# Optimization experiments

Measured on AMD Instinct MI355X. Metric: run time of the kernel, lower is better.

The kernel has to match this reference:

```python
import jax, jax.numpy as jnp
import numpy as np

D_MODEL = 1024
D_STATE = 16
DT_RANK = 64  # ceil(1024/16)
DT_MIN, DT_MAX = 1e-3, 1e-1


def setup_inputs() -> dict:
    key = jax.random.key(0)
    ks = jax.random.split(key, 6)
    x = jax.random.normal(ks[0], (2, 2048, D_MODEL), jnp.float32)
    A_log = jax.random.normal(ks[1], (D_MODEL, D_STATE), jnp.float32)
    D = jax.random.normal(ks[2], (D_MODEL,), jnp.float32)
    # nn.Linear default init ~ U(-1/sqrt(fan_in), 1/sqrt(fan_in)); normal*scale is fine for a baseline
    x_proj_w = jax.random.normal(ks[3], (DT_RANK + 2 * D_STATE, D_MODEL), jnp.float32) * (D_MODEL ** -0.5)
    dt_init_std = DT_RANK ** -0.5
    dt_proj_w = jax.random.uniform(ks[4], (D_MODEL, DT_RANK), jnp.float32, -dt_init_std, dt_init_std)
    dt = jnp.exp(jax.random.uniform(ks[5], (D_MODEL,), jnp.float32)
                 * (np.log(DT_MAX) - np.log(DT_MIN)) + np.log(DT_MIN))
    dt_proj_b = dt + jnp.log(-jnp.expm1(-dt))  # inverse-softplus init
    return {"x": x, "A_log": A_log, "D": D, "x_proj_w": x_proj_w,
            "dt_proj_w": dt_proj_w, "dt_proj_b": dt_proj_b}


def _s6(x, A_log, D, x_proj_w, dt_proj_w, dt_proj_b):
    A = -jnp.exp(A_log)                                    # (d, n)
    xp = jnp.einsum('bld,ed->ble', x, x_proj_w)            # (b, l, r+2n)
    d_rank = xp[..., :DT_RANK]
    Bm = xp[..., DT_RANK:DT_RANK + D_STATE]                # (b, l, n)
    Cm = xp[..., DT_RANK + D_STATE:]                       # (b, l, n)
    delta = jax.nn.softplus(jnp.einsum('blr,dr->bld', d_rank, dt_proj_w) + dt_proj_b)
    deltaA = jnp.exp(jnp.einsum('bld,dn->bldn', delta, A))          # (b, l, d, n)
    deltaB_u = jnp.einsum('bld,bln,bld->bldn', delta, Bm, x)        # (b, l, d, n)

    def step(h, inp):
        dA_t, dBu_t, C_t = inp          # (b,d,n), (b,d,n), (b,n)
        h = dA_t * h + dBu_t
        y = jnp.einsum('bdn,bn->bd', h, C_t)
        return h, y

    b, l, d = x.shape
    h0 = jnp.zeros((b, d, D_STATE), x.dtype)
    _, ys = jax.lax.scan(step, h0,
                         (deltaA.transpose(1, 0, 2, 3),
                          deltaB_u.transpose(1, 0, 2, 3),
                          Cm.transpose(1, 0, 2)))
    y = ys.transpose(1, 0, 2) + x * D                      # (b, l, d)
    return y


def reference(x, A_log, D, x_proj_w, dt_proj_w, dt_proj_b):
    return _s6(x, A_log, D, x_proj_w, dt_proj_w, dt_proj_b)
```

## Files before the change

### kernel.cpp

```cpp
#include <hip/hip_runtime.h>
#include <math.h>

#define Bb 2
#define Ll 2048
#define Dm 1024
#define Ns 16
#define Rr 64
#define Ee 96
#define XPS 8
#define BLK (Bb*Ll)
#define NTHR 256
#define LOG2E 1.4426950408889634f
#define LN2   0.6931471805599453f

typedef __attribute__((ext_vector_type(8))) short bf16x8;
typedef __attribute__((ext_vector_type(4))) float f32x4;

__device__ inline float ex2(float x) {
#if __has_builtin(__builtin_amdgcn_exp2f)
    return __builtin_amdgcn_exp2f(x);
#else
    return exp2f(x);
#endif
}
__device__ inline float lg2(float x) {
#if __has_builtin(__builtin_amdgcn_logf)
    return __builtin_amdgcn_logf(x);
#else
    return log2f(x);
#endif
}
__device__ inline float softplus_f(float z) {
    float e = ex2(-fabsf(z) * LOG2E);
    return fmaxf(z, 0.f) + lg2(1.f + e) * LN2;
}

__device__ inline unsigned short f2bf(float f) {
    union { float f; unsigned u; } v; v.f = f;
    unsigned u = v.u + 0x7fffu + ((v.u >> 16) & 1u);
    return (unsigned short)(u >> 16);
}
__device__ inline uint2 pack4(float a, float b, float c, float d) {
    unsigned u0 = ((unsigned)f2bf(b) << 16) | f2bf(a);
    unsigned u1 = ((unsigned)f2bf(d) << 16) | f2bf(c);
    return make_uint2(u0, u1);
}

__global__ void __launch_bounds__(NTHR, 4)
k_xproj(const float* __restrict__ x, const float* __restrict__ xw,
        float* __restrict__ xp_part) {
    __shared__ __align__(16) short sm[16*128 + 96*128];
    int tid = threadIdx.x, lane = tid & 63, wid = tid >> 6;
    int bx = blockIdx.x;
    int ks = bx & 7, mt = bx >> 3;
    int i0 = mt * 16;
    int kb = ks * 128;
    short* sA = sm;
    short* sB = sm + 16*128;

#pragma unroll
    for (int i = 0; i < 2; ++i) {
        int idx = tid + i * 256;
        int r = idx >> 5, c4 = idx & 31;
        float4 v = *(const float4*)(x + (size_t)(i0 + r) * Dm + kb + c4 * 4);
        int unit = (c4 >> 1) ^ (r & 7);
        *(uint2*)(sA + r * 128 + unit * 8 + (c4 & 1) * 4) = pack4(v.x, v.y, v.z, v.w);
    }
#pragma unroll
    for (int i = 0; i < 12; ++i) {
        int idx = tid + i * 256;
        int r = idx >> 5, c4 = idx & 31;
        float4 v = *(const float4*)(xw + (size_t)r * Dm + kb + c4 * 4);
        int unit = (c4 >> 1) ^ (r & 7);
        *(uint2*)(sB + r * 128 + unit * 8 + (c4 & 1) * 4) = pack4(v.x, v.y, v.z, v.w);
    }
    __syncthreads();

    f32x4 acc[6];
#pragma unroll
    for (int t = 0; t < 6; ++t) acc[t] = (f32x4)0.f;
    int ra = lane & 15;
    int g = wid * 4 + (lane >> 4);
    bf16x8 a = *(bf16x8*)(sA + ra * 128 + ((g ^ (ra & 7)) << 3));
#pragma unroll
    for (int nt = 0; nt < 6; ++nt) {
        int br = nt * 16 + (lane & 15);
        bf16x8 b = *(bf16x8*)(sB + br * 128 + ((g ^ (br & 7)) << 3));
        acc[nt] = __builtin_amdgcn_mfma_f32_16x16x32_bf16(a, b, acc[nt], 0, 0, 0);
    }
    __syncthreads();

    float* rp = (float*)sm;
#pragma unroll
    for (int nt = 0; nt < 6; ++nt)
#pragma unroll
        for (int j = 0; j < 4; ++j) {
            int r = ((lane >> 4) << 2) + j;
            int c = nt * 16 + (lane & 15);
            rp[wid * 1536 + r * 96 + c] = acc[nt][j];
        }
    __syncthreads();
#pragma unroll
    for (int o = 0; o < 6; ++o) {
        int idx = o * 256 + tid;
        float s = rp[idx] + rp[1536 + idx] + rp[3072 + idx] + rp[4608 + idx];
        int r = idx / 96, c = idx - r * 96;
        xp_part[((size_t)ks * BLK + (i0 + r)) * Ee + c] = s;
    }
}

__global__ void __launch_bounds__(NTHR)
k_prep(const float* __restrict__ xp_part, float* __restrict__ xp) {
    int g = blockIdx.x * NTHR + threadIdx.x;
    const float4* p = (const float4*)xp_part;
    float4 s = p[g];
#pragma unroll
    for (int i = 1; i < XPS; ++i) {
        float4 v = p[(size_t)i * (BLK * Ee / 4) + g];
        s.x += v.x; s.y += v.y; s.z += v.z; s.w += v.w;
    }
    ((float4*)xp)[g] = s;
}

__global__ void __launch_bounds__(NTHR)
k_delta(const float* __restrict__ xp, const float* __restrict__ dtw,
        const float* __restrict__ dtb, float* __restrict__ delta) {
    __shared__ __align__(16) short sA[128 * 64];
    __shared__ __align__(16) short sB[64 * 64];
    int tid = threadIdx.x, lane = tid & 63, wid = tid >> 6;
    int nt16 = blockIdx.x & 15, mt = blockIdx.x >> 4;
    int i0 = mt * 128, j0 = nt16 * 64;

#pragma unroll
    for (int i = 0; i < 8; ++i) {
        int idx = tid + i * 256;
        int r = idx >> 4, c4 = idx & 15;
        float4 v = *(const float4*)(xp + (size_t)(i0 + r) * Ee + c4 * 4);
        int unit = (c4 >> 1) ^ (r & 7);
        *(uint2*)(sA + r * 64 + unit * 8 + (c4 & 1) * 4) = pack4(v.x, v.y, v.z, v.w);
    }
#pragma unroll
    for (int i = 0; i < 4; ++i) {
        int idx = tid + i * 256;
        int r = idx >> 4, c4 = idx & 15;
        float4 v = *(const float4*)(dtw + (size_t)(j0 + r) * Rr + c4 * 4);
        int unit = (c4 >> 1) ^ (r & 7);
        *(uint2*)(sB + r * 64 + unit * 8 + (c4 & 1) * 4) = pack4(v.x, v.y, v.z, v.w);
    }
    __syncthreads();

    f32x4 acc[2][4];
#pragma unroll
    for (int m = 0; m < 2; ++m)
#pragma unroll
        for (int nt = 0; nt < 4; ++nt) acc[m][nt] = (f32x4)0.f;
    int R = wid * 32;
    int r0 = R + (lane & 15), r1 = R + 16 + (lane & 15);
#pragma unroll
    for (int ks = 0; ks < 2; ++ks) {
        int g = ks * 4 + (lane >> 4);
        bf16x8 a0 = *(bf16x8*)(sA + r0 * 64 + ((g ^ (r0 & 7)) << 3));
        bf16x8 a1 = *(bf16x8*)(sA + r1 * 64 + ((g ^ (r1 & 7)) << 3));
#pragma unroll
        for (int nt = 0; nt < 4; ++nt) {
            int br = nt * 16 + (lane & 15);
            bf16x8 b = *(bf16x8*)(sB + br * 64 + ((g ^ (br & 7)) << 3));
            acc[0][nt] = __builtin_amdgcn_mfma_f32_16x16x32_bf16(a0, b, acc[0][nt], 0, 0, 0);
            acc[1][nt] = __builtin_amdgcn_mfma_f32_16x16x32_bf16(a1, b, acc[1][nt], 0, 0, 0);
        }
    }
#pragma unroll
    for (int nt = 0; nt < 4; ++nt) {
        int col = j0 + nt * 16 + (lane & 15);
        float bias = dtb[col];
#pragma unroll
        for (int m = 0; m < 2; ++m)
#pragma unroll
            for (int j = 0; j < 4; ++j) {
                int row = i0 + R + m * 16 + ((lane >> 4) << 2) + j;
                delta[(size_t)row * Dm + col] = softplus_f(acc[m][nt][j] + bias);
            }
    }
}

__device__ inline void load_a2(const float* __restrict__ A_log, int d, float* a2) {
    const float4* Ap = (const float4*)(A_log + (size_t)d * Ns);
    float4 a0 = Ap[0], a1 = Ap[1], a2v = Ap[2], a3 = Ap[3];
    float tmp[Ns] = {a0.x,a0.y,a0.z,a0.w, a1.x,a1.y,a1.z,a1.w,
                     a2v.x,a2v.y,a2v.z,a2v.w, a3.x,a3.y,a3.z,a3.w};
#pragma unroll
    for (int n = 0; n < Ns; ++n) a2[n] = -__expf(tmp[n]) * LOG2E;
}

template<int CHv>
__global__ void __launch_bounds__(NTHR)
k_scan_part(const float* __restrict__ delta, const float* __restrict__ x,
            const float* __restrict__ xp, const float* __restrict__ A_log,
            float* __restrict__ Ec, float* __restrict__ Sc) {
    constexpr int CLv = Ll / CHv;
    int bx = blockIdx.x;
    int dblk = bx & 3, chunk = (bx >> 2) & (CHv - 1), b = bx >> 2 >> __builtin_ctz(CHv);
    int tid = threadIdx.x;
    int d = dblk * 256 + tid;
    int row0 = b * Ll + chunk * CLv;

    float a2[Ns], h[Ns];
    load_a2(A_log, d, a2);
#pragma unroll
    for (int n = 0; n < Ns; ++n) h[n] = 0.f;
    float sd = 0.f;

#pragma unroll 4
    for (int t = 0; t < CLv; ++t) {
        size_t row = (size_t)(row0 + t);
        float dl = delta[row * Dm + d];
        float xv = x[row * Dm + d];
        const float* bp = xp + row * Ee + Rr;
        float4 B0 = *(const float4*)(bp + 0),  B1 = *(const float4*)(bp + 4);
        float4 B2 = *(const float4*)(bp + 8),  B3 = *(const float4*)(bp + 12);
        float Bv[Ns] = {B0.x,B0.y,B0.z,B0.w, B1.x,B1.y,B1.z,B1.w,
                        B2.x,B2.y,B2.z,B2.w, B3.x,B3.y,B3.z,B3.w};
        float dx = dl * xv;
        sd += dl;
#pragma unroll
        for (int n = 0; n < Ns; ++n)
            h[n] = fmaf(ex2(dl * a2[n]), h[n], dx * Bv[n]);
    }
    size_t base = ((size_t)b * CHv + chunk) * Dm + d;
    float4* Ep = (float4*)(Ec + base * Ns);
    Ep[0] = make_float4(h[0],  h[1],  h[2],  h[3]);
    Ep[1] = make_float4(h[4],  h[5],  h[6],  h[7]);
    Ep[2] = make_float4(h[8],  h[9],  h[10], h[11]);
    Ep[3] = make_float4(h[12], h[13], h[14], h[15]);
    Sc[base] = sd;
}

template<int CHv, int G>
__global__ void __launch_bounds__(NTHR)
k_comb1(const float* __restrict__ Ec, const float* __restrict__ Sc,
        const float* __restrict__ A_log, float* __restrict__ Hloc,
        float* __restrict__ Spre, float* __restrict__ Eg, float* __restrict__ Sg) {
    constexpr int CPG = CHv / G;
    int gid = blockIdx.x * NTHR + threadIdx.x;
    int n = gid & (Ns - 1);
    int d = (gid >> 4) & (Dm - 1);
    int g = (gid >> 14) & (G - 1);
    int b = gid >> 17;
    float a2 = -__expf(A_log[d * Ns + n]) * LOG2E;
    float h = 0.f, S = 0.f;
#pragma unroll
    for (int j = 0; j < CPG; ++j) {
        size_t base = ((size_t)b * CHv + g * CPG + j) * Dm + d;
        float e  = Ec[base * Ns + n];
        float sc = Sc[base];
        Hloc[base * Ns + n] = h;
        if (n == 0) Spre[base] = S;
        h = fmaf(ex2(a2 * sc), h, e);
        S += sc;
    }
    size_t gb = ((size_t)b * G + g) * Dm + d;
    Eg[gb * Ns + n] = h;
    if (n == 0) Sg[gb] = S;
}

template<int G>
__global__ void __launch_bounds__(NTHR)
k_comb2(const float* __restrict__ Eg, const float* __restrict__ Sg,
        const float* __restrict__ A_log, float* __restrict__ Hg) {
    int gid = blockIdx.x * NTHR + threadIdx.x;
    int n = gid & (Ns - 1);
    int d = (gid >> 4) & (Dm - 1);
    int b = gid >> 14;
    float a2 = -__expf(A_log[d * Ns + n]) * LOG2E;
    float h = 0.f;
#pragma unroll
    for (int g = 0; g < G; ++g) {
        size_t gb = ((size_t)b * G + g) * Dm + d;
        Hg[gb * Ns + n] = h;
        h = fmaf(ex2(a2 * Sg[gb]), h, Eg[gb * Ns + n]);
    }
}

template<int CHv, int G>
__global__ void __launch_bounds__(NTHR)
k_scan_full(const float* __restrict__ delta, const float* __restrict__ x,
            const float* __restrict__ xp, const float* __restrict__ A_log,
            const float* __restrict__ Dp, const float* __restrict__ Hloc,
            const float* __restrict__ Spre, const float* __restrict__ Hg,
            float* __restrict__ out) {
    constexpr int CLv = Ll / CHv;
    constexpr int CPG = CHv / G;
    int bx = blockIdx.x;
    int dblk = bx & 3, chunk = (bx >> 2) & (CHv - 1), b = bx >> 2 >> __builtin_ctz(CHv);
    int tid = threadIdx.x;
    int d = dblk * 256 + tid;
    int row0 = b * Ll + chunk * CLv;

    float a2[Ns], h[Ns];
    load_a2(A_log, d, a2);
    size_t base = ((size_t)b * CHv + chunk) * Dm + d;
    size_t gb   = ((size_t)b * G + chunk / CPG) * Dm + d;
    {
        float sp = Spre[base];
        const float4* Hl = (const float4*)(Hloc + base * Ns);
        const float4* Hp = (const float4*)(Hg + gb * Ns);
        float4 l0 = Hl[0], l1 = Hl[1], l2 = Hl[2], l3 = Hl[3];
        float4 g0 = Hp[0], g1 = Hp[1], g2 = Hp[2], g3 = Hp[3];
        float lv[Ns] = {l0.x,l0.y,l0.z,l0.w, l1.x,l1.y,l1.z,l1.w,
                        l2.x,l2.y,l2.z,l2.w, l3.x,l3.y,l3.z,l3.w};
        float gv[Ns] = {g0.x,g0.y,g0.z,g0.w, g1.x,g1.y,g1.z,g1.w,
                        g2.x,g2.y,g2.z,g2.w, g3.x,g3.y,g3.z,g3.w};
#pragma unroll
        for (int n = 0; n < Ns; ++n) h[n] = fmaf(ex2(a2[n] * sp), gv[n], lv[n]);
    }
    float Dval = Dp[d];

#pragma unroll 4
    for (int t = 0; t < CLv; ++t) {
        size_t row = (size_t)(row0 + t);
        float dl = delta[row * Dm + d];
        float xv = x[row * Dm + d];
        const float* bp = xp + row * Ee + Rr;
        float4 B0 = *(const float4*)(bp + 0),  B1 = *(const float4*)(bp + 4);
        float4 B2 = *(const float4*)(bp + 8),  B3 = *(const float4*)(bp + 12);
        float4 C0 = *(const float4*)(bp + 16), C1 = *(const float4*)(bp + 20);
        float4 C2 = *(const float4*)(bp + 24), C3 = *(const float4*)(bp + 28);
        float Bv[Ns] = {B0.x,B0.y,B0.z,B0.w, B1.x,B1.y,B1.z,B1.w,
                        B2.x,B2.y,B2.z,B2.w, B3.x,B3.y,B3.z,B3.w};
        float Cv[Ns] = {C0.x,C0.y,C0.z,C0.w, C1.x,C1.y,C1.z,C1.w,
                        C2.x,C2.y,C2.z,C2.w, C3.x,C3.y,C3.z,C3.w};
        float dx = dl * xv;
        float ya[4] = {0.f, 0.f, 0.f, 0.f};
#pragma unroll
        for (int n = 0; n < Ns; ++n) {
            h[n] = fmaf(ex2(dl * a2[n]), h[n], dx * Bv[n]);
            ya[n & 3] = fmaf(h[n], Cv[n], ya[n & 3]);
        }
        out[row * Dm + d] = fmaf(xv, Dval, (ya[0] + ya[1]) + (ya[2] + ya[3]));
    }
}

extern "C" void kernel_launch(void* const* d_in, const int* in_sizes, int n_in,
                              void* d_out, int out_size, void* d_ws, size_t ws_size,
                              hipStream_t stream) {
    const float* x     = (const float*)d_in[0];
    const float* A_log = (const float*)d_in[1];
    const float* Dp    = (const float*)d_in[2];
    const float* xw    = (const float*)d_in[3];
    const float* dtw   = (const float*)d_in[4];
    const float* dtb   = (const float*)d_in[5];
    float* out = (float*)d_out;
    float* ws  = (float*)d_ws;

    float* xp      = ws;
    float* delta   = xp + 393216;
    float* S3      = delta + 4194304;
    float* xp_part = S3;

    k_xproj<<<dim3(2048), dim3(NTHR), 0, stream>>>(x, xw, xp_part);
    k_prep <<<dim3(384),  dim3(NTHR), 0, stream>>>(xp_part, xp);
    k_delta<<<dim3(512),  dim3(NTHR), 0, stream>>>(xp, dtw, dtb, delta);

    constexpr int G = 8;
    constexpr int CHv = 64;
    float* Ec   = S3;
    float* Sc   = Ec   + (size_t)Bb*CHv*Dm*Ns;
    float* Hloc = Sc   + (size_t)Bb*CHv*Dm;
    float* Spre = Hloc + (size_t)Bb*CHv*Dm*Ns;
    float* Eg   = Spre + (size_t)Bb*CHv*Dm;
    float* Sg   = Eg   + (size_t)Bb*G*Dm*Ns;
    float* Hg   = Sg   + (size_t)Bb*G*Dm;

    k_scan_part<CHv>  <<<dim3(Bb*CHv*4), dim3(NTHR), 0, stream>>>(delta, x, xp, A_log, Ec, Sc);
    k_comb1<CHv, G>   <<<dim3(Bb*G*Dm*Ns/NTHR), dim3(NTHR), 0, stream>>>(Ec, Sc, A_log, Hloc, Spre, Eg, Sg);
    k_comb2<G>        <<<dim3(Bb*Dm*Ns/NTHR), dim3(NTHR), 0, stream>>>(Eg, Sg, A_log, Hg);
    k_scan_full<CHv,G><<<dim3(Bb*CHv*4), dim3(NTHR), 0, stream>>>(delta, x, xp, A_log, Dp, Hloc, Spre, Hg, out);
}
```

Baseline: 137.0 us.

## Process two scan chunks per thread and stage B/C rows in shared memory

Doubles the chunk count and has each thread advance two independent chunk recurrences at once, which gives more instruction-level parallelism to hide the latency of the serial exp/fma chain. The B and C vectors for the block's rows are staged once into shared memory instead of every thread reading them from global memory. The trade-off is higher register pressure from two 16-wide state arrays per thread, an extra barrier, and a larger combine stage because there are more chunks.

New measurement: 145.7 us. +6.4%, slower.

```diff
diff --git a/kernel.cpp b/kernel.cpp
--- a/kernel.cpp
+++ b/kernel.cpp
@@ -198,41 +198,54 @@
             const float* __restrict__ xp, const float* __restrict__ A_log,
             float* __restrict__ Ec, float* __restrict__ Sc) {
     constexpr int CLv = Ll / CHv;
+    constexpr int NP = CHv / 2;
+    __shared__ __align__(16) float bsh[2 * CLv * 16];
     int bx = blockIdx.x;
-    int dblk = bx & 3, chunk = (bx >> 2) & (CHv - 1), b = bx >> 2 >> __builtin_ctz(CHv);
+    int dblk = bx & 3, cp = (bx >> 2) & (NP - 1), b = bx >> 2 >> __builtin_ctz(NP);
     int tid = threadIdx.x;
     int d = dblk * 256 + tid;
-    int row0 = b * Ll + chunk * CLv;
-
-    float a2[Ns], h[Ns];
+    int row0 = b * Ll + cp * (2 * CLv);
+
+    if (tid < 2 * CLv * 4) {
+        int r = tid >> 2, c = (tid & 3) * 4;
+        *(float4*)(bsh + r*16 + c) =
+            *(const float4*)(xp + (size_t)(row0 + r) * Ee + Rr + c);
+    }
+    float a2[Ns];
     load_a2(A_log, d, a2);
-#pragma unroll
-    for (int n = 0; n < Ns; ++n) h[n] = 0.f;
-    float sd = 0.f;
+    __syncthreads();
+
+    float h0[Ns], h1[Ns];
+#pragma unroll
+    for (int n = 0; n < Ns; ++n) { h0[n] = 0.f; h1[n] = 0.f; }
+    float sd0 = 0.f, sd1 = 0.f;
 
 #pragma unroll 4
     for (int t = 0; t < CLv; ++t) {
-        size_t row = (size_t)(row0 + t);
-        float dl = delta[row * Dm + d];
-        float xv = x[row * Dm + d];
-        const float* bp = xp + row * Ee + Rr;
-        float4 B0 = *(const float4*)(bp + 0),  B1 = *(const float4*)(bp + 4);
-        float4 B2 = *(const float4*)(bp + 8),  B3 = *(const float4*)(bp + 12);
-        float Bv[Ns] = {B0.x,B0.y,B0.z,B0.w, B1.x,B1.y,B1.z,B1.w,
-                        B2.x,B2.y,B2.z,B2.w, B3.x,B3.y,B3.z,B3.w};
-        float dx = dl * xv;
-        sd += dl;
-#pragma unroll
-        for (int n = 0; n < Ns; ++n)
-            h[n] = fmaf(ex2(dl * a2[n]), h[n], dx * Bv[n]);
-    }
-    size_t base = ((size_t)b * CHv + chunk) * Dm + d;
-    float4* Ep = (float4*)(Ec + base * Ns);
-    Ep[0] = make_float4(h[0],  h[1],  h[2],  h[3]);
-    Ep[1] = make_float4(h[4],  h[5],  h[6],  h[7]);
-    Ep[2] = make_float4(h[8],  h[9],  h[10], h[11]);
-    Ep[3] = make_float4(h[12], h[13], h[14], h[15]);
-    Sc[base] = sd;
+        size_t rA = (size_t)(row0 + t);
+        size_t rB = (size_t)(row0 + CLv + t);
+        float dl0 = delta[rA * Dm + d], xv0 = x[rA * Dm + d];
+        float dl1 = delta[rB * Dm + d], xv1 = x[rB * Dm + d];
+        const float* b0 = bsh + t * 16;
+        const float* b1 = bsh + (CLv + t) * 16;
+        float dx0 = dl0 * xv0, dx1 = dl1 * xv1;
+        sd0 += dl0; sd1 += dl1;
+#pragma unroll
+        for (int n = 0; n < Ns; ++n) {
+            h0[n] = fmaf(ex2(dl0 * a2[n]), h0[n], dx0 * b0[n]);
+            h1[n] = fmaf(ex2(dl1 * a2[n]), h1[n], dx1 * b1[n]);
+        }
+    }
+    size_t base0 = ((size_t)b * CHv + 2 * cp) * Dm + d;
+    size_t base1 = base0 + Dm;
+    float4* E0 = (float4*)(Ec + base0 * Ns);
+    float4* E1 = (float4*)(Ec + base1 * Ns);
+    E0[0] = make_float4(h0[0],h0[1],h0[2],h0[3]);   E0[1] = make_float4(h0[4],h0[5],h0[6],h0[7]);
+    E0[2] = make_float4(h0[8],h0[9],h0[10],h0[11]); E0[3] = make_float4(h0[12],h0[13],h0[14],h0[15]);
+    E1[0] = make_float4(h1[0],h1[1],h1[2],h1[3]);   E1[1] = make_float4(h1[4],h1[5],h1[6],h1[7]);
+    E1[2] = make_float4(h1[8],h1[9],h1[10],h1[11]); E1[3] = make_float4(h1[12],h1[13],h1[14],h1[15]);
+    Sc[base0] = sd0;
+    Sc[base1] = sd1;
 }
 
 template<int CHv, int G>
@@ -289,54 +302,70 @@
             const float* __restrict__ Spre, const float* __restrict__ Hg,
             float* __restrict__ out) {
     constexpr int CLv = Ll / CHv;
+    constexpr int NP = CHv / 2;
     constexpr int CPG = CHv / G;
+    __shared__ __align__(16) float bcs[2 * CLv * 32];
     int bx = blockIdx.x;
-    int dblk = bx & 3, chunk = (bx >> 2) & (CHv - 1), b = bx >> 2 >> __builtin_ctz(CHv);
+    int dblk = bx & 3, cp = (bx >> 2) & (NP - 1), b = bx >> 2 >> __builtin_ctz(NP);
     int tid = threadIdx.x;
     int d = dblk * 256 + tid;
-    int row0 = b * Ll + chunk * CLv;
-
-    float a2[Ns], h[Ns];
+    int row0 = b * Ll + cp * (2 * CLv);
+
+    {
+        int r = tid >> 3, c = (tid & 7) * 4;
+        *(float4*)(bcs + r*32 + c) =
+            *(const float4*)(xp + (size_t)(row0 + r) * Ee + Rr + c);
+    }
+    float a2[Ns];
     load_a2(A_log, d, a2);
-    size_t base = ((size_t)b * CHv + chunk) * Dm + d;
-    size_t gb   = ((size_t)b * G + chunk / CPG) * Dm + d;
+    int c0 = 2 * cp;
+    size_t base0 = ((size_t)b * CHv + c0) * Dm + d;
+    size_t base1 = base0 + Dm;
+    size_t gb    = ((size_t)b * G + c0 / CPG) * Dm + d;
+
+    float h0[Ns], h1[Ns];
     {
-        float sp = Spre[base];
-        const float4* Hl = (const float4*)(Hloc + base * Ns);
-        const float4* Hp = (const float4*)(Hg + gb * Ns);
-        float4 l0 = Hl[0], l1 = Hl[1], l2 = Hl[2], l3 = Hl[3];
-        float4 g0 = Hp[0], g1 = Hp[1], g2 = Hp[2], g3 = Hp[3];
-        float lv[Ns] = {l0.x,l0.y,l0.z,l0.w, l1.x,l1.y,l1.z,l1.w,
-                        l2.x,l2.y,l2.z,l2.w, l3.x,l3.y,l3.z,l3.w};
-        float gv[Ns] = {g0.x,g0.y,g0.z,g0.w, g1.x,g1.y,g1.z,g1.w,
-                        g2.x,g2.y,g2.z,g2.w, g3.x,g3.y,g3.z,g3.w};
-#pragma unroll
-        for (int n = 0; n < Ns; ++n) h[n] = fmaf(ex2(a2[n] * sp), gv[n], lv[n]);
+        float sp0 = Spre[base0], sp1 = Spre[base1];
+        const float4* Hl0 = (const float4*)(Hloc + base0 * Ns);
+        const float4* Hl1 = (const float4*)(Hloc + base1 * Ns);
+        const float4* Hp  = (const float4*)(Hg + gb * Ns);
+        float4 l0a = Hl0[0], l0b = Hl0[1], l0c = Hl0[2], l0d = Hl0[3];
+        float4 l1a = Hl1[0], l1b = Hl1[1], l1c = Hl1[2], l1d = Hl1[3];
+        float4 g0a = Hp[0],  g0b = Hp[1],  g0c = Hp[2],  g0d = Hp[3];
+        float lv0[Ns] = {l0a.x,l0a.y,l0a.z,l0a.w, l0b.x,l0b.y,l0b.z,l0b.w,
+                         l0c.x,l0c.y,l0c.z,l0c.w, l0d.x,l0d.y,l0d.z,l0d.w};
+        float lv1[Ns] = {l1a.x,l1a.y,l1a.z,l1a.w, l1b.x,l1b.y,l1b.z,l1b.w,
+                         l1c.x,l1c.y,l1c.z,l1c.w, l1d.x,l1d.y,l1d.z,l1d.w};
+        float gv[Ns]  = {g0a.x,g0a.y,g0a.z,g0a.w, g0b.x,g0b.y,g0b.z,g0b.w,
+                         g0c.x,g0c.y,g0c.z,g0c.w, g0d.x,g0d.y,g0d.z,g0d.w};
+#pragma unroll
+        for (int n = 0; n < Ns; ++n) {
+            h0[n] = fmaf(ex2(a2[n] * sp0), gv[n], lv0[n]);
+            h1[n] = fmaf(ex2(a2[n] * sp1), gv[n], lv1[n]);
+        }
     }
     float Dval = Dp[d];
+    __syncthreads();
 
 #pragma unroll 4
     for (int t = 0; t < CLv; ++t) {
-        size_t row = (size_t)(row0 + t);
-        float dl = delta[row * Dm + d];
-        float xv = x[row * Dm + d];
-        const float* bp = xp + row * Ee + Rr;
-        float4 B0 = *(const float4*)(bp + 0),  B1 = *(const float4*)(bp + 4);
-        float4 B2 = *(const float4*)(bp + 8),  B3 = *(const float4*)(bp + 12);
-        float4 C0 = *(const float4*)(bp + 16), C1 = *(const float4*)(bp + 20);
-        float4 C2 = *(const float4*)(bp + 24), C3 = *(const float4*)(bp + 28);
-        float Bv[Ns] = {B0.x,B0.y,B0.z,B0.w, B1.x,B1.y,B1.z,B1.w,
-                        B2.x,B2.y,B2.z,B2.w, B3.x,B3.y,B3.z,B3.w};
-        float Cv[Ns] = {C0.x,C0.y,C0.z,C0.w, C1.x,C1.y,C1.z,C1.w,
-                        C2.x,C2.y,C2.z,C2.w, C3.x,C3.y,C3.z,C3.w};
-        float dx = dl * xv;
-        float ya[4] = {0.f, 0.f, 0.f, 0.f};
+        size_t rA = (size_t)(row0 + t);
+        size_t rB = (size_t)(row0 + CLv + t);
+        float dl0 = delta[rA * Dm + d], xv0 = x[rA * Dm + d];
+        float dl1 = delta[rB * Dm + d], xv1 = x[rB * Dm + d];
+        const float* p0 = bcs + t * 32;
+        const float* p1 = bcs + (CLv + t) * 32;
+        float dx0 = dl0 * xv0, dx1 = dl1 * xv1;
+        float y0a[4] = {0.f,0.f,0.f,0.f}, y1a[4] = {0.f,0.f,0.f,0.f};
 #pragma unroll
         for (int n = 0; n < Ns; ++n) {
-            h[n] = fmaf(ex2(dl * a2[n]), h[n], dx * Bv[n]);
-            ya[n & 3] = fmaf(h[n], Cv[n], ya[n & 3]);
+            h0[n] = fmaf(ex2(dl0 * a2[n]), h0[n], dx0 * p0[n]);
+            y0a[n & 3] = fmaf(h0[n], p0[16 + n], y0a[n & 3]);
+            h1[n] = fmaf(ex2(dl1 * a2[n]), h1[n], dx1 * p1[n]);
+            y1a[n & 3] = fmaf(h1[n], p1[16 + n], y1a[n & 3]);
         }
-        out[row * Dm + d] = fmaf(xv, Dval, (ya[0] + ya[1]) + (ya[2] + ya[3]));
+        out[rA * Dm + d] = fmaf(xv0, Dval, (y0a[0] + y0a[1]) + (y0a[2] + y0a[3]));
+        out[rB * Dm + d] = fmaf(xv1, Dval, (y1a[0] + y1a[1]) + (y1a[2] + y1a[3]));
     }
 }
 
@@ -362,7 +391,7 @@
     k_delta<<<dim3(512),  dim3(NTHR), 0, stream>>>(xp, dtw, dtb, delta);
 
     constexpr int G = 8;
-    constexpr int CHv = 64;
+    constexpr int CHv = 128;
     float* Ec   = S3;
     float* Sc   = Ec   + (size_t)Bb*CHv*Dm*Ns;
     float* Hloc = Sc   + (size_t)Bb*CHv*Dm;
@@ -371,8 +400,8 @@
     float* Sg   = Eg   + (size_t)Bb*G*Dm*Ns;
     float* Hg   = Sg   + (size_t)Bb*G*Dm;
 
-    k_scan_part<CHv>  <<<dim3(Bb*CHv*4), dim3(NTHR), 0, stream>>>(delta, x, xp, A_log, Ec, Sc);
+    k_scan_part<CHv>  <<<dim3(Bb*(CHv/2)*4), dim3(NTHR), 0, stream>>>(delta, x, xp, A_log, Ec, Sc);
     k_comb1<CHv, G>   <<<dim3(Bb*G*Dm*Ns/NTHR), dim3(NTHR), 0, stream>>>(Ec, Sc, A_log, Hloc, Spre, Eg, Sg);
     k_comb2<G>        <<<dim3(Bb*Dm*Ns/NTHR), dim3(NTHR), 0, stream>>>(Eg, Sg, A_log, Hg);
-    k_scan_full<CHv,G><<<dim3(Bb*CHv*4), dim3(NTHR), 0, stream>>>(delta, x, xp, A_log, Dp, Hloc, Spre, Hg, out);
-}
+    k_scan_full<CHv,G><<<dim3(Bb*(CHv/2)*4), dim3(NTHR), 0, stream>>>(delta, x, xp, A_log, Dp, Hloc, Spre, Hg, out);
+}
```
